# Optimization experiments

Hardware: AMD Instinct MI355X
Metric: run time of the kernel (lower is better)

The kernel has to match this reference:

```python
import jax, jax.numpy as jnp
import numpy as np

N = 100000      # nodes in first graph
D = 64          # latent_size
E1 = 3200000    # edges in graph 1
M = 200000      # link-nodes (rows of pos1)
E2 = 3200000    # edges in graph 2
P2 = 200000     # len(pos2), must be even
D1 = 2          # depth1
D2 = 2          # depth2
MAXX = 1000     # max_x


def _gcn(x, edge, W, b, n):
    row, col = edge[0], edge[1]
    xw = x @ W
    deg = jax.ops.segment_sum(jnp.ones(edge.shape[1], x.dtype), col, num_segments=n) + 1.0
    dinv = jax.lax.rsqrt(deg)
    msg = xw[row] * (dinv[row] * dinv[col])[:, None]
    agg = jax.ops.segment_sum(msg, col, num_segments=n) + xw * (dinv * dinv)[:, None]
    return agg + b


def _gn(x, w, b, ms):
    # PyG GraphNorm, single graph: (x - ms*mean)/sqrt(var+eps)*w + b
    mean = jnp.mean(x, axis=0, keepdims=True)
    c = x - ms * mean
    var = jnp.mean(c * c, axis=0, keepdims=True)
    return w * c * jax.lax.rsqrt(var + 1e-5) + b


def setup_inputs() -> dict:
    key = jax.random.key(0)
    ks = jax.random.split(key, 12)
    s = 0.1
    inp = {}
    inp["x"] = jax.random.randint(ks[0], (N,), 0, MAXX + 1)
    inp["na"] = jnp.zeros((1, 1), jnp.float32)  # unused (use_node_attr=False)
    inp["edge1"] = jax.random.randint(ks[1], (2, E1), 0, N)
    inp["edge2"] = jax.random.randint(ks[2], (2, E2), 0, M)
    inp["edge2_r"] = inp["edge2"][::-1]
    inp["pos1"] = jax.random.randint(ks[3], (M, 2), 0, N)
    inp["pos2"] = jax.random.randint(ks[4], (P2,), 0, M)
    inp["emb_table"] = jax.random.normal(ks[5], (MAXX + 1, D)) * s
    inp["emb_gn_w"] = jnp.ones((D,))
    inp["emb_gn_b"] = jnp.zeros((D,))
    inp["emb_gn_ms"] = jnp.ones((D,))

    def layer_params(k, depth):
        return (jax.random.normal(k, (depth, D, D)) * s,
                jnp.zeros((depth, D)),
                jnp.ones((depth, D)),
                jnp.zeros((depth, D)),
                jnp.ones((depth, D)))

    (inp["c1_W"], inp["c1_b"], inp["c1_gn_w"], inp["c1_gn_b"], inp["c1_gn_ms"]) = layer_params(ks[6], D1)
    (inp["c2_W"], inp["c2_b"], inp["c2_gn_w"], inp["c2_gn_b"], inp["c2_gn_ms"]) = layer_params(ks[7], D2)
    (inp["c2r_W"], inp["c2r_b"], inp["c2r_gn_w"], inp["c2r_gn_b"], inp["c2r_gn_ms"]) = layer_params(ks[8], D2)
    inp["pred_W"] = jax.random.normal(ks[9], (D, 1)) * s
    inp["pred_b"] = jnp.zeros((1,))
    return inp


def reference(x, na, edge1, edge2, edge2_r, pos1, pos2,
              emb_table, emb_gn_w, emb_gn_b, emb_gn_ms,
              c1_W, c1_b, c1_gn_w, c1_gn_b, c1_gn_ms,
              c2_W, c2_b, c2_gn_w, c2_gn_b, c2_gn_ms,
              c2r_W, c2r_b, c2r_gn_w, c2r_gn_b, c2r_gn_ms,
              pred_W, pred_b):
    # embedding + GraphNorm (dropout is identity at inference)
    h = emb_table[x]
    h = _gn(h, emb_gn_w, emb_gn_b, emb_gn_ms)
    # conv1 stack on the N-node graph
    for l in range(D1):
        h = jax.nn.relu(_gn(_gcn(h, edge1, c1_W[l], c1_b[l], N),
                            c1_gn_w[l], c1_gn_b[l], c1_gn_ms[l]))
    # pairwise gather-multiply -> M link-nodes
    h = h[pos1[:, 0]] * h[pos1[:, 1]]
    # dual-branch conv2 stack on the M-node graph
    for l in range(D2):
        a = jax.nn.relu(_gn(_gcn(h, edge2, c2_W[l], c2_b[l], M),
                            c2_gn_w[l], c2_gn_b[l], c2_gn_ms[l]))
        b2 = jax.nn.relu(_gn(_gcn(h, edge2_r, c2r_W[l], c2r_b[l], M),
                             c2r_gn_w[l], c2r_gn_b[l], c2r_gn_ms[l]))
        h = a + b2
    # pos2 gather, alternating mask == even/odd interleave, product, linear head
    h = h[pos2]
    h = h[0::2] * h[1::2]
    return h @ pred_W + pred_b
```

## Files before the change

### kernel.cpp

```cpp
#include <hip/hip_runtime.h>
#include <hip/hip_fp16.h>

#define NN 100000
#define MMn 200000
#define DD 64
#define NE1 3200000
#define NE2 3200000
#define SHB 6
#define NB1 1563
#define NB2 3125
#define CAP1 2560
#define CAP2 1536
#define NBLK 128
#define GGRID 2048

static inline int cdiv_l(long a, long b) { return (int)((a + b - 1) / b); }

__global__ void fill_i32_k(int* p, int v, long n) {
    long i = (long)blockIdx.x * blockDim.x + threadIdx.x;
    long st = (long)gridDim.x * blockDim.x;
    for (; i < n; i += st) p[i] = v;
}
__global__ void fill_f32_k(float* p, float v, long n) {
    long i = (long)blockIdx.x * blockDim.x + threadIdx.x;
    long st = (long)gridDim.x * blockDim.x;
    for (; i < n; i += st) p[i] = v;
}
__global__ void ginit_k(int* gcur, int nb, int cap) {
    int b = blockIdx.x * blockDim.x + threadIdx.x;
    if (b < nb) gcur[b] = b * cap;
}
__global__ void histx_k(const int* __restrict__ x, int n, int* __restrict__ freq) {
    int i = blockIdx.x * blockDim.x + threadIdx.x;
    if (i < n) atomicAdd(&freq[x[i]], 1);
}

__global__ __launch_bounds__(256) void stage_one_k(
    const int* __restrict__ keys, const int* __restrict__ vals, int ne,
    int* __restrict__ gcur, int2* __restrict__ stg, int nb, int cap)
{
    __shared__ int lcnt[3200];
    __shared__ int lbase[3200];
    int tid = threadIdx.x;
    for (int b = tid; b < nb; b += 256) lcnt[b] = 0;
    __syncthreads();
    int chunk = (ne + (int)gridDim.x - 1) / (int)gridDim.x;
    int s = blockIdx.x * chunk, e = min(ne, s + chunk);
    for (int i = s + tid; i < e; i += 256) atomicAdd(&lcnt[keys[i] >> SHB], 1);
    __syncthreads();
    for (int b = tid; b < nb; b += 256) {
        int c = lcnt[b];
        lbase[b] = c ? atomicAdd(&gcur[b], c) : 0;
        lcnt[b] = 0;
    }
    __syncthreads();
    for (int i = s + tid; i < e; i += 256) {
        int k = keys[i];
        int bkt = k >> SHB;
        int idx = atomicAdd(&lcnt[bkt], 1);
        long pos = (long)lbase[bkt] + idx;
        if (pos < (long)(bkt + 1) * cap) stg[pos] = make_int2(vals[i], k);
    }
}

template <int CAPT>
__global__ __launch_bounds__(256) void fill_one_k(
    const int2* __restrict__ stg, const int* __restrict__ gcur, int n,
    int* __restrict__ rows, int2* __restrict__ offs, float* __restrict__ dinv)
{
    __shared__ int2 ent[CAPT];
    __shared__ int deg[64];
    __shared__ int sstart[65];
    int b = blockIdx.x, tid = threadIdx.x;
    long s = (long)b * CAPT;
    int cnt = min(gcur[b] - (int)s, CAPT);
    if (tid < 64) deg[tid] = 0;
    __syncthreads();
    for (int i = tid; i < cnt; i += 256) {
        int2 u = stg[s + i];
        ent[i] = u;
        atomicAdd(&deg[u.y & 63], 1);
    }
    __syncthreads();
    if (tid == 0) {
        int acc = 0;
#pragma unroll
        for (int j = 0; j < 64; ++j) { sstart[j] = acc; acc += deg[j]; }
        sstart[64] = acc;
    }
    __syncthreads();
    int node = (b << SHB) + tid;
    if (tid < 64 && node < n) {
        int st = sstart[tid], en = sstart[tid + 1];
        offs[node] = make_int2((int)s + st, (int)s + en);
        dinv[node] = rsqrtf((float)(en - st) + 1.0f);
    }
    if (tid < 64) deg[tid] = sstart[tid];
    __syncthreads();
    for (int i = tid; i < cnt; i += 256) {
        int2 u = ent[i];
        int idx = atomicAdd(&deg[u.y & 63], 1);
        rows[s + idx] = u.x;
    }
}

__device__ __forceinline__ void gn_coef(const float* __restrict__ stats,
                                        const float* __restrict__ w, const float* __restrict__ b,
                                        const float* __restrict__ ms, float nrows, int d,
                                        float& sc, float& sh) {
    float mean = stats[d] / nrows;
    float ex2 = stats[64 + d] / nrows;
    float m = ms[d];
    float var = ex2 - mean * mean * (2.f * m - m * m);
    float is = rsqrtf(var + 1e-5f);
    sc = is * w[d];
    sh = b[d] - m * mean * sc;
}

__global__ __launch_bounds__(256) void tabstats_k(const float* __restrict__ T, const int* __restrict__ freq,
                                                  int nv, float* __restrict__ stats) {
    __shared__ float sS[256], sQ[256];
    int tid = threadIdx.x; int d = tid & 63; int g = tid >> 6;
    float s = 0.f, q = 0.f;
    for (int v = g; v < nv; v += 4) {
        float f = (float)freq[v];
        float t = T[(long)v * DD + d];
        s += f * t; q += f * t * t;
    }
    sS[tid] = s; sQ[tid] = q; __syncthreads();
    if (tid < 128) { sS[tid] += sS[tid + 128]; sQ[tid] += sQ[tid + 128]; }
    __syncthreads();
    if (tid < 64) { stats[d] = sS[tid] + sS[tid + 64]; stats[64 + d] = sQ[tid] + sQ[tid + 64]; }
}

__global__ void tnorm_k(const float* __restrict__ T, const float* __restrict__ stats,
                        const float* __restrict__ w, const float* __restrict__ b,
                        const float* __restrict__ ms, __half* __restrict__ Tn, int nv) {
    int i = blockIdx.x * blockDim.x + threadIdx.x;
    if (i >= nv * DD) return;
    int d = i & 63;
    float sc, sh;
    gn_coef(stats, w, b, ms, (float)NN, d, sc, sh);
    Tn[i] = __float2half(fmaf(T[i], sc, sh));
}

template <int NORM>
__global__ __launch_bounds__(256) void gcn_fused_k(
    const __half* __restrict__ hsrc, const int2* __restrict__ offs,
    const int* __restrict__ rows, const float* __restrict__ dinv,
    const float* __restrict__ stats, const float* __restrict__ gw,
    const float* __restrict__ gb, const float* __restrict__ gms, float nprev,
    const float* __restrict__ W, const float* __restrict__ bias,
    __half* __restrict__ Z, float* __restrict__ ostats, int n)
{
    __shared__ float sW[4096];
    __shared__ float sP[256];
    __shared__ float rs[256];
    int tid = threadIdx.x;
    for (int i = tid; i < 4096; i += 256) sW[i] = W[i];
    int wr = tid >> 6, d = tid & 63;
    int q = tid & 31, grp = (tid >> 5) & 1;
    int d0 = q * 2;
    float sc0 = 1.f, sh0 = 0.f, sc1 = 1.f, sh1 = 0.f;
    if (NORM) {
        gn_coef(stats, gw, gb, gms, nprev, d0, sc0, sh0);
        gn_coef(stats, gw, gb, gms, nprev, d0 + 1, sc1, sh1);
    }
    float bd = bias[d];
    float sumz = 0.f, sumq = 0.f;
    const __half2* h2 = (const __half2*)hsrc;
    int ngrp = (n + 3) >> 2;
    for (int g = blockIdx.x; g < ngrp; g += gridDim.x) {
        int node = g * 4 + wr;
        float P0 = 0.f, P1 = 0.f;
        if (node < n) {
            int2 se = offs[node];
            int s = se.x, e = se.y;
            float dc = dinv[node];
            float a0 = 0.f, a1 = 0.f, b0 = 0.f, b1 = 0.f;
            if (!grp) {
                __half2 u = h2[(long)node * 32 + q];
                float x0 = __low2float(u), x1 = __high2float(u);
                if (NORM) {
                    x0 = fmaf(x0, sc0, sh0); x1 = fmaf(x1, sc1, sh1);
                    if (NORM == 2) { x0 = fmaxf(x0, 0.f); x1 = fmaxf(x1, 0.f); }
                }
                a0 = x0 * dc; a1 = x1 * dc;
            }
            int i = s + grp;
            for (; i + 2 < e; i += 4) {
                int r0 = rows[i], r1 = rows[i + 2];
                float w0 = dinv[r0], w1 = dinv[r1];
                __half2 u0 = h2[(long)r0 * 32 + q];
                __half2 u1 = h2[(long)r1 * 32 + q];
                float x00 = __low2float(u0), x01 = __high2float(u0);
                float x10 = __low2float(u1), x11 = __high2float(u1);
                if (NORM) {
                    x00 = fmaf(x00, sc0, sh0); x01 = fmaf(x01, sc1, sh1);
                    x10 = fmaf(x10, sc0, sh0); x11 = fmaf(x11, sc1, sh1);
                    if (NORM == 2) {
                        x00 = fmaxf(x00, 0.f); x01 = fmaxf(x01, 0.f);
                        x10 = fmaxf(x10, 0.f); x11 = fmaxf(x11, 0.f);
                    }
                }
                a0 = fmaf(x00, w0, a0); a1 = fmaf(x01, w0, a1);
                b0 = fmaf(x10, w1, b0); b1 = fmaf(x11, w1, b1);
            }
            if (i < e) {
                int r = rows[i];
                float w0 = dinv[r];
                __half2 u = h2[(long)r * 32 + q];
                float x0 = __low2float(u), x1 = __high2float(u);
                if (NORM) {
                    x0 = fmaf(x0, sc0, sh0); x1 = fmaf(x1, sc1, sh1);
                    if (NORM == 2) { x0 = fmaxf(x0, 0.f); x1 = fmaxf(x1, 0.f); }
                }
                a0 = fmaf(x0, w0, a0); a1 = fmaf(x1, w0, a1);
            }
            a0 += b0; a1 += b1;
            a0 += __shfl_xor(a0, 32, 64);
            a1 += __shfl_xor(a1, 32, 64);
            P0 = a0 * dc; P1 = a1 * dc;
        }
        __syncthreads();
        if (!grp) { sP[wr * 64 + d0] = P0; sP[wr * 64 + d0 + 1] = P1; }
        __syncthreads();
        if (node < n) {
            float z = bd;
#pragma unroll
            for (int k = 0; k < 64; ++k) z = fmaf(sP[wr * 64 + k], sW[k * 64 + d], z);
            Z[(long)node * DD + d] = __float2half(z);
            sumz += z; sumq += z * z;
        }
    }
    rs[tid] = sumz; __syncthreads();
    if (tid < 64) atomicAdd(&ostats[tid], rs[tid] + rs[tid + 64] + rs[tid + 128] + rs[tid + 192]);
    __syncthreads();
    rs[tid] = sumq; __syncthreads();
    if (tid < 64) atomicAdd(&ostats[64 + tid], rs[tid] + rs[tid + 64] + rs[tid + 128] + rs[tid + 192]);
}

__global__ __launch_bounds__(256) void gcn_tab_fused_k(
    const __half* __restrict__ Tn, const int* __restrict__ xidx,
    const int2* __restrict__ offs, const int* __restrict__ rows,
    const float* __restrict__ dinv,
    const float* __restrict__ W, const float* __restrict__ bias,
    __half* __restrict__ Z, float* __restrict__ ostats, int n)
{
    __shared__ float sW[4096];
    __shared__ float sP[256];
    __shared__ float rs[256];
    int tid = threadIdx.x;
    for (int i = tid; i < 4096; i += 256) sW[i] = W[i];
    int wr = tid >> 6, d = tid & 63;
    int q = tid & 31, grp = (tid >> 5) & 1;
    int d0 = q * 2;
    float bd = bias[d];
    float sumz = 0.f, sumq = 0.f;
    const __half2* t2 = (const __half2*)Tn;
    int ngrp = (n + 3) >> 2;
    for (int g = blockIdx.x; g < ngrp; g += gridDim.x) {
        int node = g * 4 + wr;
        float P0 = 0.f, P1 = 0.f;
        if (node < n) {
            int2 se = offs[node];
            int s = se.x, e = se.y;
            float dc = dinv[node];
            float a0 = 0.f, a1 = 0.f, b0 = 0.f, b1 = 0.f;
            if (!grp) {
                __half2 u = t2[(long)xidx[node] * 32 + q];
                a0 = __low2float(u) * dc; a1 = __high2float(u) * dc;
            }
            int i = s + grp;
            for (; i + 2 < e; i += 4) {
                int r0 = rows[i], r1 = rows[i + 2];
                float w0 = dinv[r0], w1 = dinv[r1];
                __half2 u0 = t2[(long)xidx[r0] * 32 + q];
                __half2 u1 = t2[(long)xidx[r1] * 32 + q];
                a0 = fmaf(__low2float(u0), w0, a0); a1 = fmaf(__high2float(u0), w0, a1);
                b0 = fmaf(__low2float(u1), w1, b0); b1 = fmaf(__high2float(u1), w1, b1);
            }
            if (i < e) {
                int r = rows[i];
                float w0 = dinv[r];
                __half2 u = t2[(long)xidx[r] * 32 + q];
                a0 = fmaf(__low2float(u), w0, a0); a1 = fmaf(__high2float(u), w0, a1);
            }
            a0 += b0; a1 += b1;
            a0 += __shfl_xor(a0, 32, 64);
            a1 += __shfl_xor(a1, 32, 64);
            P0 = a0 * dc; P1 = a1 * dc;
        }
        __syncthreads();
        if (!grp) { sP[wr * 64 + d0] = P0; sP[wr * 64 + d0 + 1] = P1; }
        __syncthreads();
        if (node < n) {
            float z = bd;
#pragma unroll
            for (int k = 0; k < 64; ++k) z = fmaf(sP[wr * 64 + k], sW[k * 64 + d], z);
            Z[(long)node * DD + d] = __float2half(z);
            sumz += z; sumq += z * z;
        }
    }
    rs[tid] = sumz; __syncthreads();
    if (tid < 64) atomicAdd(&ostats[tid], rs[tid] + rs[tid + 64] + rs[tid + 128] + rs[tid + 192]);
    __syncthreads();
    rs[tid] = sumq; __syncthreads();
    if (tid < 64) atomicAdd(&ostats[64 + tid], rs[tid] + rs[tid + 64] + rs[tid + 128] + rs[tid + 192]);
}

__global__ __launch_bounds__(256) void pair_norm_mul_k(
    const __half* __restrict__ Z2, const int* __restrict__ pos,
    const float* __restrict__ stats, const float* __restrict__ gw,
    const float* __restrict__ gb, const float* __restrict__ gms,
    __half* __restrict__ h2)
{
    int tid = threadIdx.x, wr = tid >> 6, d = tid & 63;
    int idx = blockIdx.x * 4 + wr;
    if (idx >= MMn) return;
    float sc, sh;
    gn_coef(stats, gw, gb, gms, (float)NN, d, sc, sh);
    int p0 = pos[2 * idx], p1 = pos[2 * idx + 1];
    float v0 = fmaxf(fmaf(__half2float(Z2[(long)p0 * DD + d]), sc, sh), 0.f);
    float v1 = fmaxf(fmaf(__half2float(Z2[(long)p1 * DD + d]), sc, sh), 0.f);
    h2[(long)idx * DD + d] = __float2half(v0 * v1);
}

__global__ __launch_bounds__(256) void dualadd_k(
    const __half2* __restrict__ Za, const __half2* __restrict__ Zb,
    const float* __restrict__ stA, const float* __restrict__ wA, const float* __restrict__ bA, const float* __restrict__ msA,
    const float* __restrict__ stB, const float* __restrict__ wB, const float* __restrict__ bB, const float* __restrict__ msB,
    __half2* __restrict__ hout)
{
    const long nu = (long)MMn * 32;
    int tid = threadIdx.x;
    int d0 = (2 * tid) & 63;
    float scA0, shA0, scA1, shA1, scB0, shB0, scB1, shB1;
    gn_coef(stA, wA, bA, msA, (float)MMn, d0, scA0, shA0);
    gn_coef(stA, wA, bA, msA, (float)MMn, d0 + 1, scA1, shA1);
    gn_coef(stB, wB, bB, msB, (float)MMn, d0, scB0, shB0);
    gn_coef(stB, wB, bB, msB, (float)MMn, d0 + 1, scB1, shB1);
    for (long i = (long)blockIdx.x * 256 + tid; i < nu; i += (long)gridDim.x * 256) {
        __half2 ua = Za[i], ub = Zb[i];
        float a0 = __low2float(ua), a1 = __high2float(ua);
        float c0 = __low2float(ub), c1 = __high2float(ub);
        float o0 = fmaxf(fmaf(a0, scA0, shA0), 0.f) + fmaxf(fmaf(c0, scB0, shB0), 0.f);
        float o1 = fmaxf(fmaf(a1, scA1, shA1), 0.f) + fmaxf(fmaf(c1, scB1, shB1), 0.f);
        hout[i] = __halves2half2(__float2half(o0), __float2half(o1));
    }
}

__global__ __launch_bounds__(256) void final_fused_k(
    const __half* __restrict__ Za, const __half* __restrict__ Zb,
    const int* __restrict__ pos2,
    const float* __restrict__ stA, const float* __restrict__ wA, const float* __restrict__ bA, const float* __restrict__ msA,
    const float* __restrict__ stB, const float* __restrict__ wB, const float* __restrict__ bB, const float* __restrict__ msB,
    const float* __restrict__ pw, const float* __restrict__ pb,
    float* __restrict__ out, int nout)
{
    int tid = threadIdx.x, wr = tid >> 6, d = tid & 63;
    int i = blockIdx.x * 4 + wr;
    if (i >= nout) return;
    float scA, shA, scB, shB;
    gn_coef(stA, wA, bA, msA, (float)MMn, d, scA, shA);
    gn_coef(stB, wB, bB, msB, (float)MMn, d, scB, shB);
    int p0 = pos2[2 * i], p1 = pos2[2 * i + 1];
    float v0 = fmaxf(fmaf(__half2float(Za[(long)p0 * DD + d]), scA, shA), 0.f)
             + fmaxf(fmaf(__half2float(Zb[(long)p0 * DD + d]), scB, shB), 0.f);
    float v1 = fmaxf(fmaf(__half2float(Za[(long)p1 * DD + d]), scA, shA), 0.f)
             + fmaxf(fmaf(__half2float(Zb[(long)p1 * DD + d]), scB, shB), 0.f);
    float v = v0 * v1 * pw[d];
#pragma unroll
    for (int o = 32; o > 0; o >>= 1) v += __shfl_down(v, o, 64);
    if (d == 0) out[i] = v + pb[0];
}

extern "C" void kernel_launch(void* const* d_in, const int* in_sizes, int n_in,
                              void* d_out, int out_size, void* d_ws, size_t ws_size,
                              hipStream_t stream) {
    const int* x      = (const int*)d_in[0];
    const int* edge1  = (const int*)d_in[2];
    const int* edge2  = (const int*)d_in[3];
    const int* pos1   = (const int*)d_in[5];
    const int* pos2   = (const int*)d_in[6];
    const float* emb  = (const float*)d_in[7];
    const float* egw  = (const float*)d_in[8];
    const float* egb  = (const float*)d_in[9];
    const float* egm  = (const float*)d_in[10];
    const float* c1W  = (const float*)d_in[11];
    const float* c1b  = (const float*)d_in[12];
    const float* c1gw = (const float*)d_in[13];
    const float* c1gb = (const float*)d_in[14];
    const float* c1gm = (const float*)d_in[15];
    const float* c2W  = (const float*)d_in[16];
    const float* c2b  = (const float*)d_in[17];
    const float* c2gw = (const float*)d_in[18];
    const float* c2gb = (const float*)d_in[19];
    const float* c2gm = (const float*)d_in[20];
    const float* c2rW  = (const float*)d_in[21];
    const float* c2rb  = (const float*)d_in[22];
    const float* c2rgw = (const float*)d_in[23];
    const float* c2rgb = (const float*)d_in[24];
    const float* c2rgm = (const float*)d_in[25];
    const float* predW = (const float*)d_in[26];
    const float* predb = (const float*)d_in[27];
    float* out = (float*)d_out;
    const int NV = 1001;

    char* p = (char*)d_ws;
    const long SZH = (long)MMn * DD;
    __half* BA = (__half*)p; p += SZH * 2;
    __half* BB = (__half*)p; p += SZH * 2;
    __half* BC = (__half*)p; p += SZH * 2;
    int2* stg  = (int2*)p;  p += (long)NB2 * CAP2 * 8;
    int* rows1 = (int*)p; p += (long)NB1 * CAP1 * 4;
    int* rowsA = (int*)p; p += (long)NB2 * CAP2 * 4;
    int* rowsB = (int*)p; p += (long)NB2 * CAP2 * 4;
    int2* offs1 = (int2*)p; p += (long)NN * 8;
    int2* offsA = (int2*)p; p += (long)MMn * 8;
    int2* offsB = (int2*)p; p += (long)MMn * 8;
    float* dinv1  = (float*)p; p += (long)NN * 4;
    float* dinv2  = (float*)p; p += (long)MMn * 4;
    float* dinv2r = (float*)p; p += (long)MMn * 4;
    int* gcur1 = (int*)p; p += 2048 * 4;
    int* gcurA = (int*)p; p += 4096 * 4;
    int* gcurB = (int*)p; p += 4096 * 4;
    int* freq = (int*)p; p += 1024 * 4;
    float* stats = (float*)p; p += 7 * 128 * 4;
    __half* Tn = (__half*)p; p += (long)NV * DD * 2;
    if ((size_t)(p - (char*)d_ws) > ws_size) return;

    fill_i32_k<<<4, 256, 0, stream>>>(freq, 0, 1024);
    fill_f32_k<<<1, 256, 0, stream>>>(stats, 0.f, 7 * 128);

    histx_k<<<cdiv_l(NN, 256), 256, 0, stream>>>(x, NN, freq);
    tabstats_k<<<1, 256, 0, stream>>>(emb, freq, NV, stats);
    tnorm_k<<<cdiv_l((long)NV * DD, 256), 256, 0, stream>>>(emb, stats, egw, egb, egm, Tn, NV);

    ginit_k<<<cdiv_l(NB1, 256), 256, 0, stream>>>(gcur1, NB1, CAP1);
    stage_one_k<<<NBLK, 256, 0, stream>>>(edge1 + NE1, edge1, NE1, gcur1, stg, NB1, CAP1);
    fill_one_k<CAP1><<<NB1, 256, 0, stream>>>(stg, gcur1, NN, rows1, offs1, dinv1);

    ginit_k<<<cdiv_l(NB2, 256), 256, 0, stream>>>(gcurA, NB2, CAP2);
    stage_one_k<<<NBLK, 256, 0, stream>>>(edge2 + NE2, edge2, NE2, gcurA, stg, NB2, CAP2);
    fill_one_k<CAP2><<<NB2, 256, 0, stream>>>(stg, gcurA, MMn, rowsA, offsA, dinv2);

    ginit_k<<<cdiv_l(NB2, 256), 256, 0, stream>>>(gcurB, NB2, CAP2);
    stage_one_k<<<NBLK, 256, 0, stream>>>(edge2, edge2 + NE2, NE2, gcurB, stg, NB2, CAP2);
    fill_one_k<CAP2><<<NB2, 256, 0, stream>>>(stg, gcurB, MMn, rowsB, offsB, dinv2r);

    gcn_tab_fused_k<<<GGRID, 256, 0, stream>>>(Tn, x, offs1, rows1, dinv1, c1W, c1b, BB, stats + 128, NN);

    gcn_fused_k<2><<<GGRID, 256, 0, stream>>>(BB, offs1, rows1, dinv1,
        stats + 128, c1gw, c1gb, c1gm, (float)NN, c1W + 4096, c1b + 64, BA, stats + 256, NN);

    pair_norm_mul_k<<<cdiv_l(MMn, 4), 256, 0, stream>>>(BA, pos1,
        stats + 256, c1gw + 64, c1gb + 64, c1gm + 64, BC);

    gcn_fused_k<0><<<GGRID, 256, 0, stream>>>(BC, offsA, rowsA, dinv2,
        stats, nullptr, nullptr, nullptr, 1.f, c2W, c2b, BB, stats + 384, MMn);
    gcn_fused_k<0><<<GGRID, 256, 0, stream>>>(BC, offsB, rowsB, dinv2r,
        stats, nullptr, nullptr, nullptr, 1.f, c2rW, c2rb, BA, stats + 512, MMn);
    dualadd_k<<<1024, 256, 0, stream>>>((const __half2*)BB, (const __half2*)BA,
        stats + 384, c2gw, c2gb, c2gm,
        stats + 512, c2rgw, c2rgb, c2rgm, (__half2*)BC);

    gcn_fused_k<0><<<GGRID, 256, 0, stream>>>(BC, offsA, rowsA, dinv2,
        stats, nullptr, nullptr, nullptr, 1.f, c2W + 4096, c2b + 64, BB, stats + 640, MMn);
    gcn_fused_k<0><<<GGRID, 256, 0, stream>>>(BC, offsB, rowsB, dinv2r,
        stats, nullptr, nullptr, nullptr, 1.f, c2rW + 4096, c2rb + 64, BA, stats + 768, MMn);

    final_fused_k<<<cdiv_l(out_size, 4), 256, 0, stream>>>(BB, BA, pos2,
        stats + 640, c2gw + 64, c2gb + 64, c2gm + 64,
        stats + 768, c2rgw + 64, c2rgb + 64, c2rgm + 64,
        predW, predb, out, out_size);
}
```

Measured before the change: 1.736 ms.

## Drop per-node block barriers, vectorize W matvec via float4 LDS, unroll gather deeper

Each 64-lane wavefront now writes its aggregated row to its own slice of shared memory and reads it back without block-wide barriers, because one wave owns each node. The weight matrix is repacked into float4 in LDS so the 64x64 matvec uses vector LDS reads. The edge gather loop is unrolled to four edges per half-wave with independent accumulators for more memory-level parallelism. NBLK is also doubled. Correctness relies on wave-synchronous execution of the 64-wide wavefront with no explicit barrier.

```diff
diff --git a/kernel.cpp b/kernel.cpp
--- a/kernel.cpp
+++ b/kernel.cpp
@@ -11,7 +11,7 @@
 #define NB2 3125
 #define CAP1 2560
 #define CAP2 1536
-#define NBLK 128
+#define NBLK 256
 #define GGRID 2048
 
 static inline int cdiv_l(long a, long b) { return (int)((a + b - 1) / b); }
@@ -144,6 +144,15 @@
     Tn[i] = __float2half(fmaf(T[i], sc, sh));
 }
 
+__device__ __forceinline__ void load_W4(const float* __restrict__ W, float4* sW4, int tid) {
+    for (int idx = tid; idx < 1024; idx += 256) {
+        int j = idx >> 6, dd = idx & 63;
+        int k = j * 4;
+        sW4[idx] = make_float4(W[k * 64 + dd], W[(k + 1) * 64 + dd],
+                               W[(k + 2) * 64 + dd], W[(k + 3) * 64 + dd]);
+    }
+}
+
 template <int NORM>
 __global__ __launch_bounds__(256) void gcn_fused_k(
     const __half* __restrict__ hsrc, const int2* __restrict__ offs,
@@ -153,11 +162,11 @@
     const float* __restrict__ W, const float* __restrict__ bias,
     __half* __restrict__ Z, float* __restrict__ ostats, int n)
 {
-    __shared__ float sW[4096];
+    __shared__ float4 sW4[1024];
     __shared__ float sP[256];
     __shared__ float rs[256];
     int tid = threadIdx.x;
-    for (int i = tid; i < 4096; i += 256) sW[i] = W[i];
+    load_W4(W, sW4, tid);
     int wr = tid >> 6, d = tid & 63;
     int q = tid & 31, grp = (tid >> 5) & 1;
     int d0 = q * 2;
@@ -169,15 +178,18 @@
     float bd = bias[d];
     float sumz = 0.f, sumq = 0.f;
     const __half2* h2 = (const __half2*)hsrc;
+    float2* sPw = (float2*)(sP + wr * 64);
+    const float4* sPv = (const float4*)(sP + wr * 64);
     int ngrp = (n + 3) >> 2;
+    __syncthreads();
     for (int g = blockIdx.x; g < ngrp; g += gridDim.x) {
         int node = g * 4 + wr;
-        float P0 = 0.f, P1 = 0.f;
         if (node < n) {
             int2 se = offs[node];
             int s = se.x, e = se.y;
             float dc = dinv[node];
             float a0 = 0.f, a1 = 0.f, b0 = 0.f, b1 = 0.f;
+            float c0 = 0.f, c1 = 0.f, e0 = 0.f, e1 = 0.f;
             if (!grp) {
                 __half2 u = h2[(long)node * 32 + q];
                 float x0 = __low2float(u), x1 = __high2float(u);
@@ -188,25 +200,35 @@
                 a0 = x0 * dc; a1 = x1 * dc;
             }
             int i = s + grp;
-            for (; i + 2 < e; i += 4) {
-                int r0 = rows[i], r1 = rows[i + 2];
-                float w0 = dinv[r0], w1 = dinv[r1];
+            for (; i + 6 < e; i += 8) {
+                int r0 = rows[i], r1 = rows[i + 2], r2 = rows[i + 4], r3 = rows[i + 6];
+                float w0 = dinv[r0], w1 = dinv[r1], w2 = dinv[r2], w3 = dinv[r3];
                 __half2 u0 = h2[(long)r0 * 32 + q];
                 __half2 u1 = h2[(long)r1 * 32 + q];
+                __half2 u2 = h2[(long)r2 * 32 + q];
+                __half2 u3 = h2[(long)r3 * 32 + q];
                 float x00 = __low2float(u0), x01 = __high2float(u0);
                 float x10 = __low2float(u1), x11 = __high2float(u1);
+                float x20 = __low2float(u2), x21 = __high2float(u2);
+                float x30 = __low2float(u3), x31 = __high2float(u3);
                 if (NORM) {
                     x00 = fmaf(x00, sc0, sh0); x01 = fmaf(x01, sc1, sh1);
                     x10 = fmaf(x10, sc0, sh0); x11 = fmaf(x11, sc1, sh1);
+                    x20 = fmaf(x20, sc0, sh0); x21 = fmaf(x21, sc1, sh1);
+                    x30 = fmaf(x30, sc0, sh0); x31 = fmaf(x31, sc1, sh1);
                     if (NORM == 2) {
                         x00 = fmaxf(x00, 0.f); x01 = fmaxf(x01, 0.f);
                         x10 = fmaxf(x10, 0.f); x11 = fmaxf(x11, 0.f);
+                        x20 = fmaxf(x20, 0.f); x21 = fmaxf(x21, 0.f);
+                        x30 = fmaxf(x30, 0.f); x31 = fmaxf(x31, 0.f);
                     }
                 }
                 a0 = fmaf(x00, w0, a0); a1 = fmaf(x01, w0, a1);
                 b0 = fmaf(x10, w1, b0); b1 = fmaf(x11, w1, b1);
-            }
-            if (i < e) {
+                c0 = fmaf(x20, w2, c0); c1 = fmaf(x21, w2, c1);
+                e0 = fmaf(x30, w3, e0); e1 = fmaf(x31, w3, e1);
+            }
+            for (; i < e; i += 2) {
                 int r = rows[i];
                 float w0 = dinv[r];
                 __half2 u = h2[(long)r * 32 + q];
@@ -217,22 +239,24 @@
                 }
                 a0 = fmaf(x0, w0, a0); a1 = fmaf(x1, w0, a1);
             }
-            a0 += b0; a1 += b1;
+            a0 = (a0 + b0) + (c0 + e0);
+            a1 = (a1 + b1) + (c1 + e1);
             a0 += __shfl_xor(a0, 32, 64);
             a1 += __shfl_xor(a1, 32, 64);
-            P0 = a0 * dc; P1 = a1 * dc;
-        }
-        __syncthreads();
-        if (!grp) { sP[wr * 64 + d0] = P0; sP[wr * 64 + d0 + 1] = P1; }
-        __syncthreads();
-        if (node < n) {
+            if (!grp) sPw[q] = make_float2(a0 * dc, a1 * dc);
             float z = bd;
 #pragma unroll
-            for (int k = 0; k < 64; ++k) z = fmaf(sP[wr * 64 + k], sW[k * 64 + d], z);
+            for (int j = 0; j < 16; ++j) {
+                float4 pv = sPv[j];
+                float4 wv = sW4[j * 64 + d];
+                z = fmaf(pv.x, wv.x, z); z = fmaf(pv.y, wv.y, z);
+                z = fmaf(pv.z, wv.z, z); z = fmaf(pv.w, wv.w, z);
+            }
             Z[(long)node * DD + d] = __float2half(z);
             sumz += z; sumq += z * z;
         }
     }
+    __syncthreads();
     rs[tid] = sumz; __syncthreads();
     if (tid < 64) atomicAdd(&ostats[tid], rs[tid] + rs[tid + 64] + rs[tid + 128] + rs[tid + 192]);
     __syncthreads();
@@ -247,61 +271,69 @@
     const float* __restrict__ W, const float* __restrict__ bias,
     __half* __restrict__ Z, float* __restrict__ ostats, int n)
 {
-    __shared__ float sW[4096];
+    __shared__ float4 sW4[1024];
     __shared__ float sP[256];
     __shared__ float rs[256];
     int tid = threadIdx.x;
-    for (int i = tid; i < 4096; i += 256) sW[i] = W[i];
+    load_W4(W, sW4, tid);
     int wr = tid >> 6, d = tid & 63;
     int q = tid & 31, grp = (tid >> 5) & 1;
-    int d0 = q * 2;
     float bd = bias[d];
     float sumz = 0.f, sumq = 0.f;
     const __half2* t2 = (const __half2*)Tn;
+    float2* sPw = (float2*)(sP + wr * 64);
+    const float4* sPv = (const float4*)(sP + wr * 64);
     int ngrp = (n + 3) >> 2;
+    __syncthreads();
     for (int g = blockIdx.x; g < ngrp; g += gridDim.x) {
         int node = g * 4 + wr;
-        float P0 = 0.f, P1 = 0.f;
         if (node < n) {
             int2 se = offs[node];
             int s = se.x, e = se.y;
             float dc = dinv[node];
             float a0 = 0.f, a1 = 0.f, b0 = 0.f, b1 = 0.f;
+            float c0 = 0.f, c1 = 0.f, e0 = 0.f, e1 = 0.f;
             if (!grp) {
                 __half2 u = t2[(long)xidx[node] * 32 + q];
                 a0 = __low2float(u) * dc; a1 = __high2float(u) * dc;
             }
             int i = s + grp;
-            for (; i + 2 < e; i += 4) {
-                int r0 = rows[i], r1 = rows[i + 2];
-                float w0 = dinv[r0], w1 = dinv[r1];
+            for (; i + 6 < e; i += 8) {
+                int r0 = rows[i], r1 = rows[i + 2], r2 = rows[i + 4], r3 = rows[i + 6];
+                float w0 = dinv[r0], w1 = dinv[r1], w2 = dinv[r2], w3 = dinv[r3];
                 __half2 u0 = t2[(long)xidx[r0] * 32 + q];
                 __half2 u1 = t2[(long)xidx[r1] * 32 + q];
+                __half2 u2 = t2[(long)xidx[r2] * 32 + q];
+                __half2 u3 = t2[(long)xidx[r3] * 32 + q];
                 a0 = fmaf(__low2float(u0), w0, a0); a1 = fmaf(__high2float(u0), w0, a1);
                 b0 = fmaf(__low2float(u1), w1, b0); b1 = fmaf(__high2float(u1), w1, b1);
-            }
-            if (i < e) {
+                c0 = fmaf(__low2float(u2), w2, c0); c1 = fmaf(__high2float(u2), w2, c1);
+                e0 = fmaf(__low2float(u3), w3, e0); e1 = fmaf(__high2float(u3), w3, e1);
+            }
+            for (; i < e; i += 2) {
                 int r = rows[i];
                 float w0 = dinv[r];
                 __half2 u = t2[(long)xidx[r] * 32 + q];
                 a0 = fmaf(__low2float(u), w0, a0); a1 = fmaf(__high2float(u), w0, a1);
             }
-            a0 += b0; a1 += b1;
+            a0 = (a0 + b0) + (c0 + e0);
+            a1 = (a1 + b1) + (c1 + e1);
             a0 += __shfl_xor(a0, 32, 64);
             a1 += __shfl_xor(a1, 32, 64);
-            P0 = a0 * dc; P1 = a1 * dc;
-        }
-        __syncthreads();
-        if (!grp) { sP[wr * 64 + d0] = P0; sP[wr * 64 + d0 + 1] = P1; }
-        __syncthreads();
-        if (node < n) {
+            if (!grp) sPw[q] = make_float2(a0 * dc, a1 * dc);
             float z = bd;
 #pragma unroll
-            for (int k = 0; k < 64; ++k) z = fmaf(sP[wr * 64 + k], sW[k * 64 + d], z);
+            for (int j = 0; j < 16; ++j) {
+                float4 pv = sPv[j];
+                float4 wv = sW4[j * 64 + d];
+                z = fmaf(pv.x, wv.x, z); z = fmaf(pv.y, wv.y, z);
+                z = fmaf(pv.z, wv.z, z); z = fmaf(pv.w, wv.w, z);
+            }
             Z[(long)node * DD + d] = __float2half(z);
             sumz += z; sumq += z * z;
         }
     }
+    __syncthreads();
     rs[tid] = sumz; __syncthreads();
     if (tid < 64) atomicAdd(&ostats[tid], rs[tid] + rs[tid + 64] + rs[tid + 128] + rs[tid + 192]);
     __syncthreads();
```

Measured after the change: 1.431 ms. -17.6%, faster.
